# Kernel tuning notes

Measured on AMD Instinct MI355X. Metric: run time of the kernel, lower is better.

## Reference

```python
import jax, jax.numpy as jnp
import numpy as np

HALF_STEP = 0.05
NUM_V = 10  # clamp(floor(0.5/0.05), 2, 1000)
EPS = 1e-6


def _normalize(x):
    return x / (jnp.linalg.norm(x, axis=-1, keepdims=True) + EPS)


def _ragged_structure(edge_points_np):
    # Concrete (numpy) ragged-grid index structure: per-edge horizontal sample
    # counts from edge length, exclusive-cumsum offsets, repeat_interleave ids.
    sp = edge_points_np[:, 0]
    cd = edge_points_np[:, 1] - sp
    cl = np.linalg.norm(cd + EPS, axis=1)
    num_h = np.clip((cl // HALF_STEP).astype(np.int64), 2, 1000)  # [N]
    total_x = int(num_h.sum())
    begin = np.concatenate([[0], np.cumsum(num_h)[:-1]])           # roll-based exclusive cumsum
    eid_x = np.repeat(np.arange(len(num_h)), num_h)                # [total_x] edge id per x-sample
    pos_x = np.arange(total_x) - begin[eid_x]                      # dx integer position within edge
    eid = np.repeat(eid_x, NUM_V)                                  # [P] edge id per sample point
    pos_x_full = np.repeat(pos_x, NUM_V).astype(np.float32)        # coords_x integer part
    dy_idx = np.tile(np.arange(NUM_V), total_x).astype(np.float32) # coords_y integer part
    denom_full = np.repeat((num_h - 1)[eid_x], NUM_V).astype(np.float32)
    return (jnp.asarray(eid), jnp.asarray(pos_x_full), jnp.asarray(denom_full),
            jnp.asarray(dy_idx))


def _sample_img(img, uv):
    # img [1,3,H,W]; uv [P,2] in [0,1) -> bilinear sample (align_corners style)
    im = img[0]
    H, W = im.shape[1], im.shape[2]
    x = uv[:, 0] * (W - 1)
    y = uv[:, 1] * (H - 1)
    x0 = jnp.floor(x).astype(jnp.int32)
    y0 = jnp.floor(y).astype(jnp.int32)
    x1 = jnp.clip(x0 + 1, 0, W - 1)
    y1 = jnp.clip(y0 + 1, 0, H - 1)
    wx = (x - x0)[None]
    wy = (y - y0)[None]
    g = lambda yy, xx: im[:, yy, xx]  # [3,P] gather
    out = (g(y0, x0) * (1 - wx) * (1 - wy) + g(y0, x1) * wx * (1 - wy)
           + g(y1, x0) * (1 - wx) * wy + g(y1, x1) * wx * wy)
    return out.T  # [P,3]


def _forward(edge_points, intrinsic1, intrinsic2, extrinsic1, extrinsic2,
             rgb1, rgb2, eid, pos_x, denom, dy_idx):
    start = edge_points[:, 0]
    cur_dir = edge_points[:, 1] - start
    next_dir = edge_points[:, 3] - edge_points[:, 1]
    prev_dir = edge_points[:, 0] - edge_points[:, 2]
    cur_len = jnp.linalg.norm(cur_dir + EPS, axis=1)
    cur_dir = cur_dir / cur_len[:, None]
    cur_normal = _normalize(jnp.cross(cur_dir, next_dir))
    flip = cur_normal[:, 2] > 0  # dot with (0,0,1) > 0 -> flip sign
    cur_normal = jnp.where(flip[:, None], -cur_normal, cur_normal)
    cur_up = _normalize(jnp.cross(cur_normal, cur_dir))
    prev_normal = _normalize(jnp.cross(prev_dir, cur_dir))

    # ragged per-edge sample grid (repeat_interleave realized via gather on eid)
    coords_x = pos_x / denom * cur_len[eid]          # [P]
    coords_y = dy_idx / (NUM_V - 1) * 0.5            # [P]
    pts = (cur_dir[eid] * coords_x[:, None]
           + cur_up[eid] * coords_y[:, None]
           + start[eid])                              # [P,3]

    # view 1 projection + bilinear sample
    uv1 = pts @ intrinsic1.T
    uv1 = jnp.clip(uv1[:, :2] / uv1[:, 2:3], 0.0, 0.999999)
    s1 = _sample_img(rgb1, uv1)

    # view 2: K2_homog @ E2 @ inv(E1) applied to homogeneous points
    K2h = jnp.eye(4, dtype=pts.dtype).at[:3, :3].set(intrinsic2)
    T = K2h @ extrinsic2 @ jnp.linalg.inv(extrinsic1)
    ph = jnp.concatenate([pts, jnp.ones_like(pts[:, :1])], axis=1)
    uv2 = ph @ T.T
    uv2 = jnp.clip(uv2[:, :2] / uv2[:, 2:3], 0.0, 0.999999)
    s2 = _sample_img(rgb2, uv2)

    similarity_loss = jnp.mean((s1 - s2) ** 2)
    normal_loss = jnp.mean(1.0 - jnp.sum(cur_normal * prev_normal, axis=1)) / 2.0
    obs_normal = _normalize(jnp.cross(edge_points[:, 0], edge_points[:, 1]))
    snp = jnp.minimum(jnp.abs(jnp.sum(cur_up * obs_normal, axis=1)), 0.5)
    normalization_loss = jnp.mean(1.0 - snp / 0.5)
    return jnp.stack([similarity_loss, normal_loss, normalization_loss])


def setup_inputs() -> dict:
    key = jax.random.key(0)
    k0, k1, k2 = jax.random.split(key, 3)
    N, H, W = 10000, 1500, 2000
    # camera-space edge endpoints/neighbors, pushed in front of the camera
    edge_points = jax.random.normal(k0, (N, 4, 3), dtype=jnp.float32) \
        + jnp.array([0.0, 0.0, 6.0], dtype=jnp.float32)
    intrinsic1 = jnp.array([[0.3, 0.0, 0.5], [0.0, 0.3, 0.5], [0.0, 0.0, 1.0]],
                           dtype=jnp.float32)
    intrinsic2 = intrinsic1
    extrinsic1 = jnp.eye(4, dtype=jnp.float32)
    extrinsic2 = jnp.eye(4, dtype=jnp.float32).at[:3, 3].set(
        jnp.array([0.1, 0.0, 0.0], dtype=jnp.float32))
    rgb1 = jax.random.uniform(k1, (1, 3, H, W), dtype=jnp.float32)
    rgb2 = jax.random.uniform(k2, (1, 3, H, W), dtype=jnp.float32)
    return {"edge_points": edge_points, "intrinsic1": intrinsic1,
            "intrinsic2": intrinsic2, "extrinsic1": extrinsic1,
            "extrinsic2": extrinsic2, "rgb1": rgb1, "rgb2": rgb2}


def reference(edge_points, intrinsic1, intrinsic2, extrinsic1, extrinsic2,
              rgb1, rgb2):
    eid, pos_x, denom, dy_idx = _ragged_structure(np.asarray(edge_points))
    return _forward(edge_points, intrinsic1, intrinsic2, extrinsic1,
                    extrinsic2, rgb1, rgb2, eid, pos_x, denom, dy_idx)
```

## Files before the change

### kernel.cpp

```cpp
#include <hip/hip_runtime.h>
#include <math.h>

#define EPSF 1e-6f
#define NUM_V 10
#define W_IMG 2000
#define H_IMG 1500
#define HW_IMG (W_IMG * H_IMG)
#define TH_QUAD (H_IMG - 1)
#define SAMPLE_BLOCKS 2048
#define NPART (SAMPLE_BLOCKS * 4)
#define MAX_CHUNKS 80
#define RPB_P 2048

struct Ctrl {
    int cursor;
    int pad0, pad1, pad2;
    double accNL;
    double accZL;
    double accC;
};

__device__ __forceinline__ void cross3(const float a[3], const float b[3], float c[3]) {
    c[0] = a[1] * b[2] - a[2] * b[1];
    c[1] = a[2] * b[0] - a[0] * b[2];
    c[2] = a[0] * b[1] - a[1] * b[0];
}
__device__ __forceinline__ float dot3(const float a[3], const float b[3]) {
    return a[0] * b[0] + a[1] * b[1] + a[2] * b[2];
}
__device__ __forceinline__ float norm3(const float a[3]) {
    return sqrtf(a[0] * a[0] + a[1] * a[1] + a[2] * a[2]);
}

__device__ void make_T(const float* __restrict__ K2, const float* __restrict__ E1,
                       const float* __restrict__ E2, float* __restrict__ T) {
    float M[4][8];
    for (int i = 0; i < 4; ++i)
        for (int j = 0; j < 4; ++j) {
            M[i][j] = E1[i * 4 + j];
            M[i][j + 4] = (i == j) ? 1.f : 0.f;
        }
    for (int col = 0; col < 4; ++col) {
        int piv = col;
        float best = fabsf(M[col][col]);
        for (int r = col + 1; r < 4; ++r) {
            float v = fabsf(M[r][col]);
            if (v > best) { best = v; piv = r; }
        }
        if (piv != col)
            for (int j = 0; j < 8; ++j) {
                float t = M[col][j]; M[col][j] = M[piv][j]; M[piv][j] = t;
            }
        float d = 1.f / M[col][col];
        for (int j = 0; j < 8; ++j) M[col][j] *= d;
        for (int r = 0; r < 4; ++r) {
            if (r == col) continue;
            float f = M[r][col];
            for (int j = 0; j < 8; ++j) M[r][j] -= f * M[col][j];
        }
    }
    float E[4][4];
    for (int i = 0; i < 4; ++i)
        for (int j = 0; j < 4; ++j) {
            float s = 0.f;
            for (int k = 0; k < 4; ++k) s += E2[i * 4 + k] * M[k][j + 4];
            E[i][j] = s;
        }
    for (int i = 0; i < 4; ++i)
        for (int j = 0; j < 4; ++j) {
            float s;
            if (i < 3) {
                s = 0.f;
                for (int k = 0; k < 3; ++k) s += K2[i * 3 + k] * E[k][j];
            } else {
                s = E[3][j];
            }
            T[i * 4 + j] = s;
        }
}

__device__ __forceinline__ unsigned quant565(float r, float g, float b) {
    unsigned r5 = (unsigned)fmaf(r, 31.f, 0.5f);
    unsigned g6 = (unsigned)fmaf(g, 63.f, 0.5f);
    unsigned b5 = (unsigned)fmaf(b, 31.f, 0.5f);
    return (r5 << 11) | (g6 << 5) | b5;
}

__global__ __launch_bounds__(256, 8) void prep_kernel(
    const float* __restrict__ ep, int N, int GB,
    const float* __restrict__ K2v, const float* __restrict__ E1, const float* __restrict__ E2,
    const float* __restrict__ rgb1, const float* __restrict__ rgb2,
    float* __restrict__ T, Ctrl* __restrict__ ctrl,
    float4* __restrict__ geo, unsigned* __restrict__ sched,
    unsigned* __restrict__ t1, unsigned* __restrict__ t2) {
    const int b = blockIdx.x;
    if (b < RPB_P) {
        const int gpi = TH_QUAD * (W_IMG / 4);
        for (int t = b * 256 + threadIdx.x; t < 2 * gpi; t += RPB_P * 256) {
            const int img = t >= gpi;
            const int g = t - img * gpi;
            const int y = g / (W_IMG / 4);
            const int x = (g - y * (W_IMG / 4)) * 4;
            const float* src = img ? rgb2 : rgb1;
            unsigned* dst = img ? t2 : t1;
            float4 r0[3], r1[3];
#pragma unroll
            for (int c = 0; c < 3; ++c) {
                const float* bp = src + (size_t)c * HW_IMG + (size_t)y * W_IMG + x;
                r0[c] = *(const float4*)bp;
                r1[c] = *(const float4*)(bp + W_IMG);
            }
            const float* f0r = (const float*)&r0[0]; const float* f1r = (const float*)&r1[0];
            const float* f0g = (const float*)&r0[1]; const float* f1g = (const float*)&r1[1];
            const float* f0b = (const float*)&r0[2]; const float* f1b = (const float*)&r1[2];
            unsigned w[4];
#pragma unroll
            for (int k = 0; k < 4; ++k) {
                unsigned lo = quant565(f0r[k], f0g[k], f0b[k]);
                unsigned hi = quant565(f1r[k], f1g[k], f1b[k]);
                w[k] = lo | (hi << 16);
            }
            *(uint4*)(dst + (size_t)y * W_IMG + x) = make_uint4(w[0], w[1], w[2], w[3]);
        }
        return;
    }
    if (b < RPB_P + GB) {
        const int e = (b - RPB_P) * 256 + threadIdx.x;
        float nl = 0.f, zl = 0.f;
        int cn = 0;
        if (e < N) {
            const float4* P4 = (const float4*)(ep + (size_t)e * 12);
            float4 a4 = P4[0], b4 = P4[1], c4 = P4[2];
            float p0[3] = {a4.x, a4.y, a4.z};
            float p1[3] = {a4.w, b4.x, b4.y};
            float p2[3] = {b4.z, b4.w, c4.x};
            float p3[3] = {c4.y, c4.z, c4.w};
            float cd[3] = {p1[0] - p0[0], p1[1] - p0[1], p1[2] - p0[2]};
            float nd[3] = {p3[0] - p1[0], p3[1] - p1[1], p3[2] - p1[2]};
            float pd[3] = {p0[0] - p2[0], p0[1] - p2[1], p0[2] - p2[2]};
            float ce[3] = {cd[0] + EPSF, cd[1] + EPSF, cd[2] + EPSF};
            float clen = norm3(ce);
            float dir[3] = {cd[0] / clen, cd[1] / clen, cd[2] / clen};
            float cnv[3];
            cross3(dir, nd, cnv);
            float n1 = norm3(cnv) + EPSF;
            cnv[0] /= n1; cnv[1] /= n1; cnv[2] /= n1;
            if (cnv[2] > 0.f) { cnv[0] = -cnv[0]; cnv[1] = -cnv[1]; cnv[2] = -cnv[2]; }
            float up[3];
            cross3(cnv, dir, up);
            float n2 = norm3(up) + EPSF;
            up[0] /= n2; up[1] /= n2; up[2] /= n2;
            float pn[3];
            cross3(pd, dir, pn);
            float n3 = norm3(pn) + EPSF;
            pn[0] /= n3; pn[1] /= n3; pn[2] /= n3;
            float obs[3];
            cross3(p0, p1, obs);
            float n4 = norm3(obs) + EPSF;
            obs[0] /= n4; obs[1] /= n4; obs[2] /= n4;
            int nh = (int)floorf(clen / 0.05f);
            nh = max(2, min(1000, nh));
            nl = 1.f - dot3(cnv, pn);
            float snp = fminf(fabsf(dot3(up, obs)), 0.5f);
            zl = 1.f - snp * 2.f;
            const int nsamp = nh * NUM_V;
            cn = nsamp;
            geo[3 * e + 0] = make_float4(p0[0], p0[1], p0[2], clen);
            geo[3 * e + 1] = make_float4(dir[0], dir[1], dir[2], (float)(nh - 1));
            geo[3 * e + 2] = make_float4(up[0], up[1], up[2], __int_as_float(nsamp));
            const int nc = (nsamp + 127) / 128;
            const int basee = atomicAdd(&ctrl->cursor, nc);
            const unsigned tag = ((unsigned)e) << 8;
            for (int j = 0; j < nc; ++j) sched[basee + j] = tag | (unsigned)j;
        }
#pragma unroll
        for (int off = 32; off > 0; off >>= 1) {
            nl += __shfl_down(nl, off);
            zl += __shfl_down(zl, off);
            cn += __shfl_down(cn, off);
        }
        if ((threadIdx.x & 63) == 0) {
            atomicAdd(&ctrl->accNL, (double)nl);
            atomicAdd(&ctrl->accZL, (double)zl);
            atomicAdd(&ctrl->accC, (double)cn);
        }
        return;
    }
    if (threadIdx.x == 0) make_T(K2v, E1, E2, T);
}

__device__ __forceinline__ float mse565(unsigned qa0, unsigned qa1, unsigned qb0, unsigned qb1,
                                        float wxa, float wya, float wxb, float wyb) {
    float wa00 = (1.f - wxa) * (1.f - wya), wa01 = wxa * (1.f - wya);
    float wa10 = (1.f - wxa) * wya, wa11 = wxa * wya;
    float wb00 = (1.f - wxb) * (1.f - wyb), wb01 = wxb * (1.f - wyb);
    float wb10 = (1.f - wxb) * wyb, wb11 = wxb * wyb;
    unsigned a00 = qa0 & 0xffffu, a10 = qa0 >> 16, a01 = qa1 & 0xffffu, a11 = qa1 >> 16;
    unsigned b00 = qb0 & 0xffffu, b10 = qb0 >> 16, b01 = qb1 & 0xffffu, b11 = qb1 >> 16;
    float ra = fmaf((float)(a00 >> 11), wa00, fmaf((float)(a01 >> 11), wa01,
               fmaf((float)(a10 >> 11), wa10, (float)(a11 >> 11) * wa11)));
    float rb = fmaf((float)(b00 >> 11), wb00, fmaf((float)(b01 >> 11), wb01,
               fmaf((float)(b10 >> 11), wb10, (float)(b11 >> 11) * wb11)));
    float ga = fmaf((float)((a00 >> 5) & 63u), wa00, fmaf((float)((a01 >> 5) & 63u), wa01,
               fmaf((float)((a10 >> 5) & 63u), wa10, (float)((a11 >> 5) & 63u) * wa11)));
    float gb = fmaf((float)((b00 >> 5) & 63u), wb00, fmaf((float)((b01 >> 5) & 63u), wb01,
               fmaf((float)((b10 >> 5) & 63u), wb10, (float)((b11 >> 5) & 63u) * wb11)));
    float ba = fmaf((float)(a00 & 31u), wa00, fmaf((float)(a01 & 31u), wa01,
               fmaf((float)(a10 & 31u), wa10, (float)(a11 & 31u) * wa11)));
    float bb = fmaf((float)(b00 & 31u), wb00, fmaf((float)(b01 & 31u), wb01,
               fmaf((float)(b10 & 31u), wb10, (float)(b11 & 31u) * wb11)));
    float dr = (ra - rb) * (1.f / 31.f);
    float dg = (ga - gb) * (1.f / 63.f);
    float db = (ba - bb) * (1.f / 31.f);
    return fmaf(dr, dr, fmaf(dg, dg, db * db));
}

__global__ __launch_bounds__(256, 8) void sample_kernel(
    const float4* __restrict__ geo, const float* __restrict__ K1, const float* __restrict__ T,
    const unsigned* __restrict__ im1, const unsigned* __restrict__ im2,
    const unsigned* __restrict__ sched, const int* __restrict__ total_p,
    double* __restrict__ part) {
    const int wid = blockIdx.x * 4 + (threadIdx.x >> 6);
    const int lane = threadIdx.x & 63;
    const int nw = gridDim.x * 4;
    const int total = *total_p;

    const float k00 = K1[0], k01 = K1[1], k02 = K1[2];
    const float k10 = K1[3], k11 = K1[4], k12 = K1[5];
    const float k20 = K1[6], k21 = K1[7], k22 = K1[8];
    const float t00 = T[0], t01 = T[1], t02 = T[2], t03 = T[3];
    const float t10 = T[4], t11 = T[5], t12 = T[6], t13 = T[7];
    const float t20 = T[8], t21 = T[9], t22 = T[10], t23 = T[11];

    float lsum = 0.f;
    for (int base = wid; base < total; base += 2 * nw) {
        const int idxB = base + nw;
        const bool has2 = idxB < total;
        const unsigned sA = (unsigned)__builtin_amdgcn_readfirstlane((int)sched[base]);
        const unsigned sB =
            has2 ? (unsigned)__builtin_amdgcn_readfirstlane((int)sched[idxB]) : sA;
        const int eA = (int)(sA >> 8), kA = (int)(sA & 255u);
        const int eB = (int)(sB >> 8), kB = (int)(sB & 255u);
        const float4 a0 = geo[3 * eA + 0], a1 = geo[3 * eA + 1], a2 = geo[3 * eA + 2];
        const float4 b0 = geo[3 * eB + 0], b1 = geo[3 * eB + 1], b2 = geo[3 * eB + 2];
        const int nsA = __float_as_int(a2.w), nsB = __float_as_int(b2.w);
        const float lodA = a0.w * __builtin_amdgcn_rcpf(a1.w);
        const float lodB = b0.w * __builtin_amdgcn_rcpf(b1.w);

        int off1[4], off2[4];
        float wx1[4], wy1[4], wx2[4], wy2[4];
        bool ok[4];
#pragma unroll
        for (int j = 0; j < 4; ++j) {
            const int d = j >> 1, h = j & 1;
            const float4 g0 = d ? b0 : a0;
            const float4 g1 = d ? b1 : a1;
            const float4 g2 = d ? b2 : a2;
            const int ns = d ? nsB : nsA;
            const int kk = d ? kB : kA;
            const float lod = d ? lodB : lodA;
            const int i = kk * 128 + h * 64 + lane;
            ok[j] = (i < ns) && (d == 0 || has2);
            const int ic = min(i, ns - 1);
            int px = ic / NUM_V;
            int dy = ic - px * NUM_V;
            float cx = (float)px * lod;
            float cy = (float)dy * (0.5f / 9.0f);
            float X = fmaf(g1.x, cx, fmaf(g2.x, cy, g0.x));
            float Y = fmaf(g1.y, cx, fmaf(g2.y, cy, g0.y));
            float Z = fmaf(g1.z, cx, fmaf(g2.z, cy, g0.z));
            float iw1 = __builtin_amdgcn_rcpf(fmaf(k20, X, fmaf(k21, Y, k22 * Z)));
            float u1 = fminf(fmaxf(fmaf(k00, X, fmaf(k01, Y, k02 * Z)) * iw1, 0.f), 0.999999f);
            float v1 = fminf(fmaxf(fmaf(k10, X, fmaf(k11, Y, k12 * Z)) * iw1, 0.f), 0.999999f);
            float iw2 = __builtin_amdgcn_rcpf(fmaf(t20, X, fmaf(t21, Y, fmaf(t22, Z, t23))));
            float u2 = fminf(
                fmaxf(fmaf(t00, X, fmaf(t01, Y, fmaf(t02, Z, t03))) * iw2, 0.f), 0.999999f);
            float v2 = fminf(
                fmaxf(fmaf(t10, X, fmaf(t11, Y, fmaf(t12, Z, t13))) * iw2, 0.f), 0.999999f);
            float xa = u1 * (float)(W_IMG - 1), ya = v1 * (float)(H_IMG - 1);
            float xb = u2 * (float)(W_IMG - 1), yb = v2 * (float)(H_IMG - 1);
            float fxa = floorf(xa), fya = floorf(ya), fxb = floorf(xb), fyb = floorf(yb);
            off1[j] = (int)fya * W_IMG + (int)fxa;
            off2[j] = (int)fyb * W_IMG + (int)fxb;
            wx1[j] = xa - fxa; wy1[j] = ya - fya;
            wx2[j] = xb - fxb; wy2[j] = yb - fyb;
        }
        unsigned q1a[4], q1b[4], q2a[4], q2b[4];
#pragma unroll
        for (int j = 0; j < 4; ++j) { q1a[j] = im1[off1[j]]; q1b[j] = im1[off1[j] + 1]; }
#pragma unroll
        for (int j = 0; j < 4; ++j) { q2a[j] = im2[off2[j]]; q2b[j] = im2[off2[j] + 1]; }
#pragma unroll
        for (int j = 0; j < 4; ++j) {
            float v = mse565(q1a[j], q1b[j], q2a[j], q2b[j], wx1[j], wy1[j], wx2[j], wy2[j]);
            lsum += ok[j] ? v : 0.f;
        }
    }
    double dsum = (double)lsum;
#pragma unroll
    for (int off = 32; off > 0; off >>= 1) dsum += __shfl_down(dsum, off);
    if (lane == 0) part[wid] = dsum;
}

__global__ __launch_bounds__(256) void finalize_kernel(const double* __restrict__ part, int NP,
                                                       const Ctrl* __restrict__ ctrl, int N,
                                                       float* __restrict__ out) {
    __shared__ double s_s[4];
    double s = 0.0;
    for (int i = threadIdx.x; i < NP; i += 256) s += part[i];
#pragma unroll
    for (int off = 32; off > 0; off >>= 1) s += __shfl_down(s, off);
    const int wave = threadIdx.x >> 6;
    if ((threadIdx.x & 63) == 0) s_s[wave] = s;
    __syncthreads();
    if (threadIdx.x == 0) {
        double S = s_s[0] + s_s[1] + s_s[2] + s_s[3];
        double A = ctrl->accNL;
        double B = ctrl->accZL;
        double C = ctrl->accC;
        out[0] = (float)(S / (C * 3.0));
        out[1] = (float)(A / (double)N * 0.5);
        out[2] = (float)(B / (double)N);
    }
}

extern "C" void kernel_launch(void* const* d_in, const int* in_sizes, int n_in, void* d_out,
                              int out_size, void* d_ws, size_t ws_size, hipStream_t stream) {
    const float* ep = (const float*)d_in[0];
    const float* K1 = (const float*)d_in[1];
    const float* K2 = (const float*)d_in[2];
    const float* E1 = (const float*)d_in[3];
    const float* E2 = (const float*)d_in[4];
    const float* rgb1 = (const float*)d_in[5];
    const float* rgb2 = (const float*)d_in[6];
    float* out = (float*)d_out;
    const int N = in_sizes[0] / 12;

    const int GB = (N + 255) / 256;

    char* p = (char*)d_ws;
    float* T = (float*)p;               p += 256;
    Ctrl* ctrl = (Ctrl*)p;              p += 256;
    float4* geo = (float4*)p;           p += (size_t)3 * N * sizeof(float4);
    p = (char*)(((size_t)p + 255) & ~(size_t)255);
    double* part = (double*)p;          p += (size_t)NPART * sizeof(double);
    p = (char*)(((size_t)p + 255) & ~(size_t)255);
    unsigned* sched = (unsigned*)p;     p += (size_t)N * MAX_CHUNKS * sizeof(unsigned);
    p = (char*)(((size_t)p + 255) & ~(size_t)255);
    unsigned* img1 = (unsigned*)p;
    unsigned* img2 = img1 + (size_t)TH_QUAD * W_IMG;

    hipMemsetAsync(ctrl, 0, sizeof(Ctrl), stream);
    prep_kernel<<<RPB_P + GB + 1, 256, 0, stream>>>(ep, N, GB, K2, E1, E2, rgb1, rgb2, T,
                                                    ctrl, geo, sched, img1, img2);
    sample_kernel<<<SAMPLE_BLOCKS, 256, 0, stream>>>(geo, K1, T, img1, img2, sched,
                                                     &ctrl->cursor, part);
    finalize_kernel<<<1, 256, 0, stream>>>(part, NPART, ctrl, N, out);
}
```

Before: 167.5 us.

## Fuse prep, sample and finalize into one persistent kernel with grid barrier

Merges the memset, prep, sample and finalize launches into a single persistent kernel. A software grid barrier built on a global atomic counter separates the prep phase from the sampling phase, and a last-block-done counter runs the final reduction. The last block also resets the global counters, so no memset launch is needed. This removes three launch and inter-kernel gaps, but the barrier depends on all 2040 blocks being resident at once, which can deadlock if occupancy is insufficient, and prep work is now spread across blocks differently.

```diff
diff --git a/kernel.cpp b/kernel.cpp
--- a/kernel.cpp
+++ b/kernel.cpp
@@ -7,18 +7,22 @@
 #define H_IMG 1500
 #define HW_IMG (W_IMG * H_IMG)
 #define TH_QUAD (H_IMG - 1)
-#define SAMPLE_BLOCKS 2048
-#define NPART (SAMPLE_BLOCKS * 4)
+#define NBLK 2040
+#define NPART (NBLK * 4)
 #define MAX_CHUNKS 80
-#define RPB_P 2048
 
 struct Ctrl {
     int cursor;
-    int pad0, pad1, pad2;
+    int pad;
     double accNL;
     double accZL;
     double accC;
 };
+__device__ Ctrl g_ctrl;
+__device__ int g_sync0;
+__device__ int g_sync1;
+__device__ float g_T[16];
+__device__ double g_part[NPART];
 
 __device__ __forceinline__ void cross3(const float a[3], const float b[3], float c[3]) {
     c[0] = a[1] * b[2] - a[2] * b[1];
@@ -86,46 +90,47 @@
     return (r5 << 11) | (g6 << 5) | b5;
 }
 
-__global__ __launch_bounds__(256, 8) void prep_kernel(
+__device__ __forceinline__ float mse565(unsigned qa0, unsigned qa1, unsigned qb0, unsigned qb1,
+                                        float wxa, float wya, float wxb, float wyb) {
+    float wa00 = (1.f - wxa) * (1.f - wya), wa01 = wxa * (1.f - wya);
+    float wa10 = (1.f - wxa) * wya, wa11 = wxa * wya;
+    float wb00 = (1.f - wxb) * (1.f - wyb), wb01 = wxb * (1.f - wyb);
+    float wb10 = (1.f - wxb) * wyb, wb11 = wxb * wyb;
+    unsigned a00 = qa0 & 0xffffu, a10 = qa0 >> 16, a01 = qa1 & 0xffffu, a11 = qa1 >> 16;
+    unsigned b00 = qb0 & 0xffffu, b10 = qb0 >> 16, b01 = qb1 & 0xffffu, b11 = qb1 >> 16;
+    float ra = fmaf((float)(a00 >> 11), wa00, fmaf((float)(a01 >> 11), wa01,
+               fmaf((float)(a10 >> 11), wa10, (float)(a11 >> 11) * wa11)));
+    float rb = fmaf((float)(b00 >> 11), wb00, fmaf((float)(b01 >> 11), wb01,
+               fmaf((float)(b10 >> 11), wb10, (float)(b11 >> 11) * wb11)));
+    float ga = fmaf((float)((a00 >> 5) & 63u), wa00, fmaf((float)((a01 >> 5) & 63u), wa01,
+               fmaf((float)((a10 >> 5) & 63u), wa10, (float)((a11 >> 5) & 63u) * wa11)));
+    float gb = fmaf((float)((b00 >> 5) & 63u), wb00, fmaf((float)((b01 >> 5) & 63u), wb01,
+               fmaf((float)((b10 >> 5) & 63u), wb10, (float)((b11 >> 5) & 63u) * wb11)));
+    float ba = fmaf((float)(a00 & 31u), wa00, fmaf((float)(a01 & 31u), wa01,
+               fmaf((float)(a10 & 31u), wa10, (float)(a11 & 31u) * wa11)));
+    float bb = fmaf((float)(b00 & 31u), wb00, fmaf((float)(b01 & 31u), wb01,
+               fmaf((float)(b10 & 31u), wb10, (float)(b11 & 31u) * wb11)));
+    float dr = (ra - rb) * (1.f / 31.f);
+    float dg = (ga - gb) * (1.f / 63.f);
+    float db = (ba - bb) * (1.f / 31.f);
+    return fmaf(dr, dr, fmaf(dg, dg, db * db));
+}
+
+__global__ __launch_bounds__(256, 8) void mega_kernel(
     const float* __restrict__ ep, int N, int GB,
-    const float* __restrict__ K2v, const float* __restrict__ E1, const float* __restrict__ E2,
+    const float* __restrict__ K1, const float* __restrict__ K2v,
+    const float* __restrict__ E1, const float* __restrict__ E2,
     const float* __restrict__ rgb1, const float* __restrict__ rgb2,
-    float* __restrict__ T, Ctrl* __restrict__ ctrl,
     float4* __restrict__ geo, unsigned* __restrict__ sched,
-    unsigned* __restrict__ t1, unsigned* __restrict__ t2) {
+    unsigned* __restrict__ t1, unsigned* __restrict__ t2,
+    float* __restrict__ out) {
     const int b = blockIdx.x;
-    if (b < RPB_P) {
-        const int gpi = TH_QUAD * (W_IMG / 4);
-        for (int t = b * 256 + threadIdx.x; t < 2 * gpi; t += RPB_P * 256) {
-            const int img = t >= gpi;
-            const int g = t - img * gpi;
-            const int y = g / (W_IMG / 4);
-            const int x = (g - y * (W_IMG / 4)) * 4;
-            const float* src = img ? rgb2 : rgb1;
-            unsigned* dst = img ? t2 : t1;
-            float4 r0[3], r1[3];
-#pragma unroll
-            for (int c = 0; c < 3; ++c) {
-                const float* bp = src + (size_t)c * HW_IMG + (size_t)y * W_IMG + x;
-                r0[c] = *(const float4*)bp;
-                r1[c] = *(const float4*)(bp + W_IMG);
-            }
-            const float* f0r = (const float*)&r0[0]; const float* f1r = (const float*)&r1[0];
-            const float* f0g = (const float*)&r0[1]; const float* f1g = (const float*)&r1[1];
-            const float* f0b = (const float*)&r0[2]; const float* f1b = (const float*)&r1[2];
-            unsigned w[4];
-#pragma unroll
-            for (int k = 0; k < 4; ++k) {
-                unsigned lo = quant565(f0r[k], f0g[k], f0b[k]);
-                unsigned hi = quant565(f1r[k], f1g[k], f1b[k]);
-                w[k] = lo | (hi << 16);
-            }
-            *(uint4*)(dst + (size_t)y * W_IMG + x) = make_uint4(w[0], w[1], w[2], w[3]);
-        }
-        return;
-    }
-    if (b < RPB_P + GB) {
-        const int e = (b - RPB_P) * 256 + threadIdx.x;
+    const int tid = threadIdx.x;
+
+    if (b == NBLK - 1 && tid == 0) make_T(K2v, E1, E2, g_T);
+
+    if (b < GB) {
+        const int e = b * 256 + tid;
         float nl = 0.f, zl = 0.f;
         int cn = 0;
         if (e < N) {
@@ -169,7 +174,7 @@
             geo[3 * e + 1] = make_float4(dir[0], dir[1], dir[2], (float)(nh - 1));
             geo[3 * e + 2] = make_float4(up[0], up[1], up[2], __int_as_float(nsamp));
             const int nc = (nsamp + 127) / 128;
-            const int basee = atomicAdd(&ctrl->cursor, nc);
+            const int basee = atomicAdd(&g_ctrl.cursor, nc);
             const unsigned tag = ((unsigned)e) << 8;
             for (int j = 0; j < nc; ++j) sched[basee + j] = tag | (unsigned)j;
         }
@@ -179,58 +184,63 @@
             zl += __shfl_down(zl, off);
             cn += __shfl_down(cn, off);
         }
-        if ((threadIdx.x & 63) == 0) {
-            atomicAdd(&ctrl->accNL, (double)nl);
-            atomicAdd(&ctrl->accZL, (double)zl);
-            atomicAdd(&ctrl->accC, (double)cn);
-        }
-        return;
-    }
-    if (threadIdx.x == 0) make_T(K2v, E1, E2, T);
-}
-
-__device__ __forceinline__ float mse565(unsigned qa0, unsigned qa1, unsigned qb0, unsigned qb1,
-                                        float wxa, float wya, float wxb, float wyb) {
-    float wa00 = (1.f - wxa) * (1.f - wya), wa01 = wxa * (1.f - wya);
-    float wa10 = (1.f - wxa) * wya, wa11 = wxa * wya;
-    float wb00 = (1.f - wxb) * (1.f - wyb), wb01 = wxb * (1.f - wyb);
-    float wb10 = (1.f - wxb) * wyb, wb11 = wxb * wyb;
-    unsigned a00 = qa0 & 0xffffu, a10 = qa0 >> 16, a01 = qa1 & 0xffffu, a11 = qa1 >> 16;
-    unsigned b00 = qb0 & 0xffffu, b10 = qb0 >> 16, b01 = qb1 & 0xffffu, b11 = qb1 >> 16;
-    float ra = fmaf((float)(a00 >> 11), wa00, fmaf((float)(a01 >> 11), wa01,
-               fmaf((float)(a10 >> 11), wa10, (float)(a11 >> 11) * wa11)));
-    float rb = fmaf((float)(b00 >> 11), wb00, fmaf((float)(b01 >> 11), wb01,
-               fmaf((float)(b10 >> 11), wb10, (float)(b11 >> 11) * wb11)));
-    float ga = fmaf((float)((a00 >> 5) & 63u), wa00, fmaf((float)((a01 >> 5) & 63u), wa01,
-               fmaf((float)((a10 >> 5) & 63u), wa10, (float)((a11 >> 5) & 63u) * wa11)));
-    float gb = fmaf((float)((b00 >> 5) & 63u), wb00, fmaf((float)((b01 >> 5) & 63u), wb01,
-               fmaf((float)((b10 >> 5) & 63u), wb10, (float)((b11 >> 5) & 63u) * wb11)));
-    float ba = fmaf((float)(a00 & 31u), wa00, fmaf((float)(a01 & 31u), wa01,
-               fmaf((float)(a10 & 31u), wa10, (float)(a11 & 31u) * wa11)));
-    float bb = fmaf((float)(b00 & 31u), wb00, fmaf((float)(b01 & 31u), wb01,
-               fmaf((float)(b10 & 31u), wb10, (float)(b11 & 31u) * wb11)));
-    float dr = (ra - rb) * (1.f / 31.f);
-    float dg = (ga - gb) * (1.f / 63.f);
-    float db = (ba - bb) * (1.f / 31.f);
-    return fmaf(dr, dr, fmaf(dg, dg, db * db));
-}
-
-__global__ __launch_bounds__(256, 8) void sample_kernel(
-    const float4* __restrict__ geo, const float* __restrict__ K1, const float* __restrict__ T,
-    const unsigned* __restrict__ im1, const unsigned* __restrict__ im2,
-    const unsigned* __restrict__ sched, const int* __restrict__ total_p,
-    double* __restrict__ part) {
-    const int wid = blockIdx.x * 4 + (threadIdx.x >> 6);
-    const int lane = threadIdx.x & 63;
-    const int nw = gridDim.x * 4;
-    const int total = *total_p;
+        if ((tid & 63) == 0) {
+            atomicAdd(&g_ctrl.accNL, (double)nl);
+            atomicAdd(&g_ctrl.accZL, (double)zl);
+            atomicAdd(&g_ctrl.accC, (double)cn);
+        }
+    }
+
+    {
+        const int gpi = TH_QUAD * (W_IMG / 4);
+        for (int t = b * 256 + tid; t < 2 * gpi; t += NBLK * 256) {
+            const int img = t >= gpi;
+            const int g = t - img * gpi;
+            const int y = g / (W_IMG / 4);
+            const int x = (g - y * (W_IMG / 4)) * 4;
+            const float* src = img ? rgb2 : rgb1;
+            unsigned* dst = img ? t2 : t1;
+            float4 r0[3], r1[3];
+#pragma unroll
+            for (int c = 0; c < 3; ++c) {
+                const float* bp = src + (size_t)c * HW_IMG + (size_t)y * W_IMG + x;
+                r0[c] = *(const float4*)bp;
+                r1[c] = *(const float4*)(bp + W_IMG);
+            }
+            const float* f0r = (const float*)&r0[0]; const float* f1r = (const float*)&r1[0];
+            const float* f0g = (const float*)&r0[1]; const float* f1g = (const float*)&r1[1];
+            const float* f0b = (const float*)&r0[2]; const float* f1b = (const float*)&r1[2];
+            unsigned w[4];
+#pragma unroll
+            for (int k = 0; k < 4; ++k) {
+                unsigned lo = quant565(f0r[k], f0g[k], f0b[k]);
+                unsigned hi = quant565(f1r[k], f1g[k], f1b[k]);
+                w[k] = lo | (hi << 16);
+            }
+            *(uint4*)(dst + (size_t)y * W_IMG + x) = make_uint4(w[0], w[1], w[2], w[3]);
+        }
+    }
+
+    __syncthreads();
+    if (tid == 0) {
+        __threadfence();
+        __hip_atomic_fetch_add(&g_sync0, 1, __ATOMIC_ACQ_REL, __HIP_MEMORY_SCOPE_AGENT);
+        while (__hip_atomic_load(&g_sync0, __ATOMIC_ACQUIRE, __HIP_MEMORY_SCOPE_AGENT) < NBLK)
+            __builtin_amdgcn_s_sleep(2);
+    }
+    __syncthreads();
+
+    const int wid = b * 4 + (tid >> 6);
+    const int lane = tid & 63;
+    const int nw = NBLK * 4;
+    const int total = g_ctrl.cursor;
 
     const float k00 = K1[0], k01 = K1[1], k02 = K1[2];
     const float k10 = K1[3], k11 = K1[4], k12 = K1[5];
     const float k20 = K1[6], k21 = K1[7], k22 = K1[8];
-    const float t00 = T[0], t01 = T[1], t02 = T[2], t03 = T[3];
-    const float t10 = T[4], t11 = T[5], t12 = T[6], t13 = T[7];
-    const float t20 = T[8], t21 = T[9], t22 = T[10], t23 = T[11];
+    const float t00 = g_T[0], t01 = g_T[1], t02 = g_T[2], t03 = g_T[3];
+    const float t10 = g_T[4], t11 = g_T[5], t12 = g_T[6], t13 = g_T[7];
+    const float t20 = g_T[8], t21 = g_T[9], t22 = g_T[10], t23 = g_T[11];
 
     float lsum = 0.f;
     for (int base = wid; base < total; base += 2 * nw) {
@@ -287,9 +297,9 @@
         }
         unsigned q1a[4], q1b[4], q2a[4], q2b[4];
 #pragma unroll
-        for (int j = 0; j < 4; ++j) { q1a[j] = im1[off1[j]]; q1b[j] = im1[off1[j] + 1]; }
-#pragma unroll
-        for (int j = 0; j < 4; ++j) { q2a[j] = im2[off2[j]]; q2b[j] = im2[off2[j] + 1]; }
+        for (int j = 0; j < 4; ++j) { q1a[j] = t1[off1[j]]; q1b[j] = t1[off1[j] + 1]; }
+#pragma unroll
+        for (int j = 0; j < 4; ++j) { q2a[j] = t2[off2[j]]; q2b[j] = t2[off2[j] + 1]; }
 #pragma unroll
         for (int j = 0; j < 4; ++j) {
             float v = mse565(q1a[j], q1b[j], q2a[j], q2b[j], wx1[j], wy1[j], wx2[j], wy2[j]);
@@ -299,28 +309,41 @@
     double dsum = (double)lsum;
 #pragma unroll
     for (int off = 32; off > 0; off >>= 1) dsum += __shfl_down(dsum, off);
-    if (lane == 0) part[wid] = dsum;
-}
-
-__global__ __launch_bounds__(256) void finalize_kernel(const double* __restrict__ part, int NP,
-                                                       const Ctrl* __restrict__ ctrl, int N,
-                                                       float* __restrict__ out) {
+    if (lane == 0) g_part[wid] = dsum;
+
+    __shared__ int s_last;
     __shared__ double s_s[4];
+    __syncthreads();
+    if (tid == 0) {
+        __threadfence();
+        int prev = __hip_atomic_fetch_add(&g_sync1, 1, __ATOMIC_ACQ_REL,
+                                          __HIP_MEMORY_SCOPE_AGENT);
+        s_last = (prev == NBLK - 1) ? 1 : 0;
+    }
+    __syncthreads();
+    if (!s_last) return;
+
     double s = 0.0;
-    for (int i = threadIdx.x; i < NP; i += 256) s += part[i];
+    for (int i = tid; i < NPART; i += 256) s += g_part[i];
 #pragma unroll
     for (int off = 32; off > 0; off >>= 1) s += __shfl_down(s, off);
-    const int wave = threadIdx.x >> 6;
-    if ((threadIdx.x & 63) == 0) s_s[wave] = s;
-    __syncthreads();
-    if (threadIdx.x == 0) {
+    if ((tid & 63) == 0) s_s[tid >> 6] = s;
+    __syncthreads();
+    if (tid == 0) {
         double S = s_s[0] + s_s[1] + s_s[2] + s_s[3];
-        double A = ctrl->accNL;
-        double B = ctrl->accZL;
-        double C = ctrl->accC;
+        double A = g_ctrl.accNL;
+        double B = g_ctrl.accZL;
+        double C = g_ctrl.accC;
         out[0] = (float)(S / (C * 3.0));
         out[1] = (float)(A / (double)N * 0.5);
         out[2] = (float)(B / (double)N);
+        g_ctrl.cursor = 0;
+        g_ctrl.accNL = 0.0;
+        g_ctrl.accZL = 0.0;
+        g_ctrl.accC = 0.0;
+        __hip_atomic_store(&g_sync0, 0, __ATOMIC_RELAXED, __HIP_MEMORY_SCOPE_AGENT);
+        __hip_atomic_store(&g_sync1, 0, __ATOMIC_RELEASE, __HIP_MEMORY_SCOPE_AGENT);
+        __threadfence();
     }
 }
 
@@ -339,21 +362,13 @@
     const int GB = (N + 255) / 256;
 
     char* p = (char*)d_ws;
-    float* T = (float*)p;               p += 256;
-    Ctrl* ctrl = (Ctrl*)p;              p += 256;
     float4* geo = (float4*)p;           p += (size_t)3 * N * sizeof(float4);
-    p = (char*)(((size_t)p + 255) & ~(size_t)255);
-    double* part = (double*)p;          p += (size_t)NPART * sizeof(double);
     p = (char*)(((size_t)p + 255) & ~(size_t)255);
     unsigned* sched = (unsigned*)p;     p += (size_t)N * MAX_CHUNKS * sizeof(unsigned);
     p = (char*)(((size_t)p + 255) & ~(size_t)255);
     unsigned* img1 = (unsigned*)p;
     unsigned* img2 = img1 + (size_t)TH_QUAD * W_IMG;
 
-    hipMemsetAsync(ctrl, 0, sizeof(Ctrl), stream);
-    prep_kernel<<<RPB_P + GB + 1, 256, 0, stream>>>(ep, N, GB, K2, E1, E2, rgb1, rgb2, T,
-                                                    ctrl, geo, sched, img1, img2);
-    sample_kernel<<<SAMPLE_BLOCKS, 256, 0, stream>>>(geo, K1, T, img1, img2, sched,
-                                                     &ctrl->cursor, part);
-    finalize_kernel<<<1, 256, 0, stream>>>(part, NPART, ctrl, N, out);
-}
+    mega_kernel<<<NBLK, 256, 0, stream>>>(ep, N, GB, K1, K2, E1, E2, rgb1, rgb2,
+                                          geo, sched, img1, img2, out);
+}
```

New measurement: 585.9 us. 250% more time.

## Precompute per-edge projected pixel-space affine coefficients and drop control memset

Applied to the files above, without the earlier changes.

Per-edge geometry is folded with both camera projections (K1 and the precomputed T) and the image scale in the prep kernel. The sampler then evaluates each sample as two small affine combinations plus a reciprocal instead of a 3D point build followed by two full projections. The control block moves to a __device__ global that finalize resets, which removes the hipMemsetAsync launch. In exchange the per-edge record grows from 3 to 6 float4, so the sampler reads more geometry per chunk, and every prep edge block recomputes T into shared memory.

```diff
diff --git a/kernel.cpp b/kernel.cpp
--- a/kernel.cpp
+++ b/kernel.cpp
@@ -11,14 +11,17 @@
 #define NPART (SAMPLE_BLOCKS * 4)
 #define MAX_CHUNKS 80
 #define RPB_P 2048
+#define XCLAMP (0.999999f * (float)(W_IMG - 1))
+#define YCLAMP (0.999999f * (float)(H_IMG - 1))
 
 struct Ctrl {
     int cursor;
-    int pad0, pad1, pad2;
+    int pad;
     double accNL;
     double accZL;
     double accC;
 };
+__device__ Ctrl g_ctrl;
 
 __device__ __forceinline__ void cross3(const float a[3], const float b[3], float c[3]) {
     c[0] = a[1] * b[2] - a[2] * b[1];
@@ -88,9 +91,9 @@
 
 __global__ __launch_bounds__(256, 8) void prep_kernel(
     const float* __restrict__ ep, int N, int GB,
-    const float* __restrict__ K2v, const float* __restrict__ E1, const float* __restrict__ E2,
+    const float* __restrict__ K1, const float* __restrict__ K2v,
+    const float* __restrict__ E1, const float* __restrict__ E2,
     const float* __restrict__ rgb1, const float* __restrict__ rgb2,
-    float* __restrict__ T, Ctrl* __restrict__ ctrl,
     float4* __restrict__ geo, unsigned* __restrict__ sched,
     unsigned* __restrict__ t1, unsigned* __restrict__ t2) {
     const int b = blockIdx.x;
@@ -125,6 +128,9 @@
         return;
     }
     if (b < RPB_P + GB) {
+        __shared__ float sT[16];
+        if (threadIdx.x == 0) make_T(K2v, E1, E2, sT);
+        __syncthreads();
         const int e = (b - RPB_P) * 256 + threadIdx.x;
         float nl = 0.f, zl = 0.f;
         int cn = 0;
@@ -165,11 +171,34 @@
             zl = 1.f - snp * 2.f;
             const int nsamp = nh * NUM_V;
             cn = nsamp;
-            geo[3 * e + 0] = make_float4(p0[0], p0[1], p0[2], clen);
-            geo[3 * e + 1] = make_float4(dir[0], dir[1], dir[2], (float)(nh - 1));
-            geo[3 * e + 2] = make_float4(up[0], up[1], up[2], __int_as_float(nsamp));
+
+            const float lod = clen / (float)(nh - 1);
+            float dlx[3] = {dir[0] * lod, dir[1] * lod, dir[2] * lod};
+            const float cyc = 0.5f / 9.0f;
+            float upc[3] = {up[0] * cyc, up[1] * cyc, up[2] * cyc};
+            const float Wm1 = (float)(W_IMG - 1), Hm1 = (float)(H_IMG - 1);
+            float k0[3] = {K1[0], K1[1], K1[2]};
+            float k1r[3] = {K1[3], K1[4], K1[5]};
+            float k2[3] = {K1[6], K1[7], K1[8]};
+            float T0[3] = {sT[0], sT[1], sT[2]};
+            float T1[3] = {sT[4], sT[5], sT[6]};
+            float T2[3] = {sT[8], sT[9], sT[10]};
+            geo[6 * e + 0] = make_float4(dot3(k0, dlx) * Wm1, dot3(k1r, dlx) * Hm1,
+                                         dot3(k2, dlx), __int_as_float(nsamp));
+            geo[6 * e + 1] = make_float4(dot3(k0, upc) * Wm1, dot3(k1r, upc) * Hm1,
+                                         dot3(k2, upc), 0.f);
+            geo[6 * e + 2] = make_float4(dot3(k0, p0) * Wm1, dot3(k1r, p0) * Hm1,
+                                         dot3(k2, p0), 0.f);
+            geo[6 * e + 3] = make_float4(dot3(T0, dlx) * Wm1, dot3(T1, dlx) * Hm1,
+                                         dot3(T2, dlx), 0.f);
+            geo[6 * e + 4] = make_float4(dot3(T0, upc) * Wm1, dot3(T1, upc) * Hm1,
+                                         dot3(T2, upc), 0.f);
+            geo[6 * e + 5] = make_float4((dot3(T0, p0) + sT[3]) * Wm1,
+                                         (dot3(T1, p0) + sT[7]) * Hm1,
+                                         dot3(T2, p0) + sT[11], 0.f);
+
             const int nc = (nsamp + 127) / 128;
-            const int basee = atomicAdd(&ctrl->cursor, nc);
+            const int basee = atomicAdd(&g_ctrl.cursor, nc);
             const unsigned tag = ((unsigned)e) << 8;
             for (int j = 0; j < nc; ++j) sched[basee + j] = tag | (unsigned)j;
         }
@@ -180,13 +209,11 @@
             cn += __shfl_down(cn, off);
         }
         if ((threadIdx.x & 63) == 0) {
-            atomicAdd(&ctrl->accNL, (double)nl);
-            atomicAdd(&ctrl->accZL, (double)zl);
-            atomicAdd(&ctrl->accC, (double)cn);
-        }
-        return;
-    }
-    if (threadIdx.x == 0) make_T(K2v, E1, E2, T);
+            atomicAdd(&g_ctrl.accNL, (double)nl);
+            atomicAdd(&g_ctrl.accZL, (double)zl);
+            atomicAdd(&g_ctrl.accC, (double)cn);
+        }
+    }
 }
 
 __device__ __forceinline__ float mse565(unsigned qa0, unsigned qa1, unsigned qb0, unsigned qb1,
@@ -216,21 +243,13 @@
 }
 
 __global__ __launch_bounds__(256, 8) void sample_kernel(
-    const float4* __restrict__ geo, const float* __restrict__ K1, const float* __restrict__ T,
+    const float4* __restrict__ geo,
     const unsigned* __restrict__ im1, const unsigned* __restrict__ im2,
-    const unsigned* __restrict__ sched, const int* __restrict__ total_p,
-    double* __restrict__ part) {
+    const unsigned* __restrict__ sched, double* __restrict__ part) {
     const int wid = blockIdx.x * 4 + (threadIdx.x >> 6);
     const int lane = threadIdx.x & 63;
     const int nw = gridDim.x * 4;
-    const int total = *total_p;
-
-    const float k00 = K1[0], k01 = K1[1], k02 = K1[2];
-    const float k10 = K1[3], k11 = K1[4], k12 = K1[5];
-    const float k20 = K1[6], k21 = K1[7], k22 = K1[8];
-    const float t00 = T[0], t01 = T[1], t02 = T[2], t03 = T[3];
-    const float t10 = T[4], t11 = T[5], t12 = T[6], t13 = T[7];
-    const float t20 = T[8], t21 = T[9], t22 = T[10], t23 = T[11];
+    const int total = g_ctrl.cursor;
 
     float lsum = 0.f;
     for (int base = wid; base < total; base += 2 * nw) {
@@ -241,11 +260,9 @@
             has2 ? (unsigned)__builtin_amdgcn_readfirstlane((int)sched[idxB]) : sA;
         const int eA = (int)(sA >> 8), kA = (int)(sA & 255u);
         const int eB = (int)(sB >> 8), kB = (int)(sB & 255u);
-        const float4 a0 = geo[3 * eA + 0], a1 = geo[3 * eA + 1], a2 = geo[3 * eA + 2];
-        const float4 b0 = geo[3 * eB + 0], b1 = geo[3 * eB + 1], b2 = geo[3 * eB + 2];
-        const int nsA = __float_as_int(a2.w), nsB = __float_as_int(b2.w);
-        const float lodA = a0.w * __builtin_amdgcn_rcpf(a1.w);
-        const float lodB = b0.w * __builtin_amdgcn_rcpf(b1.w);
+        const float4* gA = &geo[6 * eA];
+        const float4* gB = &geo[6 * eB];
+        const int nsA = __float_as_int(gA[0].w), nsB = __float_as_int(gB[0].w);
 
         int off1[4], off2[4];
         float wx1[4], wy1[4], wx2[4], wy2[4];
@@ -253,32 +270,29 @@
 #pragma unroll
         for (int j = 0; j < 4; ++j) {
             const int d = j >> 1, h = j & 1;
-            const float4 g0 = d ? b0 : a0;
-            const float4 g1 = d ? b1 : a1;
-            const float4 g2 = d ? b2 : a2;
+            const float4* g = d ? gB : gA;
             const int ns = d ? nsB : nsA;
             const int kk = d ? kB : kA;
-            const float lod = d ? lodB : lodA;
             const int i = kk * 128 + h * 64 + lane;
             ok[j] = (i < ns) && (d == 0 || has2);
             const int ic = min(i, ns - 1);
             int px = ic / NUM_V;
             int dy = ic - px * NUM_V;
-            float cx = (float)px * lod;
-            float cy = (float)dy * (0.5f / 9.0f);
-            float X = fmaf(g1.x, cx, fmaf(g2.x, cy, g0.x));
-            float Y = fmaf(g1.y, cx, fmaf(g2.y, cy, g0.y));
-            float Z = fmaf(g1.z, cx, fmaf(g2.z, cy, g0.z));
-            float iw1 = __builtin_amdgcn_rcpf(fmaf(k20, X, fmaf(k21, Y, k22 * Z)));
-            float u1 = fminf(fmaxf(fmaf(k00, X, fmaf(k01, Y, k02 * Z)) * iw1, 0.f), 0.999999f);
-            float v1 = fminf(fmaxf(fmaf(k10, X, fmaf(k11, Y, k12 * Z)) * iw1, 0.f), 0.999999f);
-            float iw2 = __builtin_amdgcn_rcpf(fmaf(t20, X, fmaf(t21, Y, fmaf(t22, Z, t23))));
-            float u2 = fminf(
-                fmaxf(fmaf(t00, X, fmaf(t01, Y, fmaf(t02, Z, t03))) * iw2, 0.f), 0.999999f);
-            float v2 = fminf(
-                fmaxf(fmaf(t10, X, fmaf(t11, Y, fmaf(t12, Z, t13))) * iw2, 0.f), 0.999999f);
-            float xa = u1 * (float)(W_IMG - 1), ya = v1 * (float)(H_IMG - 1);
-            float xb = u2 * (float)(W_IMG - 1), yb = v2 * (float)(H_IMG - 1);
+            const float fpx = (float)px, fdy = (float)dy;
+            const float4 s0 = g[0], s1 = g[1], s2 = g[2];
+            float u1n = fmaf(fpx, s0.x, fmaf(fdy, s1.x, s2.x));
+            float v1n = fmaf(fpx, s0.y, fmaf(fdy, s1.y, s2.y));
+            float w1  = fmaf(fpx, s0.z, fmaf(fdy, s1.z, s2.z));
+            const float4 s3 = g[3], s4 = g[4], s5 = g[5];
+            float u2n = fmaf(fpx, s3.x, fmaf(fdy, s4.x, s5.x));
+            float v2n = fmaf(fpx, s3.y, fmaf(fdy, s4.y, s5.y));
+            float w2  = fmaf(fpx, s3.z, fmaf(fdy, s4.z, s5.z));
+            float iw1 = __builtin_amdgcn_rcpf(w1);
+            float iw2 = __builtin_amdgcn_rcpf(w2);
+            float xa = fminf(fmaxf(u1n * iw1, 0.f), XCLAMP);
+            float ya = fminf(fmaxf(v1n * iw1, 0.f), YCLAMP);
+            float xb = fminf(fmaxf(u2n * iw2, 0.f), XCLAMP);
+            float yb = fminf(fmaxf(v2n * iw2, 0.f), YCLAMP);
             float fxa = floorf(xa), fya = floorf(ya), fxb = floorf(xb), fyb = floorf(yb);
             off1[j] = (int)fya * W_IMG + (int)fxa;
             off2[j] = (int)fyb * W_IMG + (int)fxb;
@@ -303,8 +317,7 @@
 }
 
 __global__ __launch_bounds__(256) void finalize_kernel(const double* __restrict__ part, int NP,
-                                                       const Ctrl* __restrict__ ctrl, int N,
-                                                       float* __restrict__ out) {
+                                                       int N, float* __restrict__ out) {
     __shared__ double s_s[4];
     double s = 0.0;
     for (int i = threadIdx.x; i < NP; i += 256) s += part[i];
@@ -315,12 +328,16 @@
     __syncthreads();
     if (threadIdx.x == 0) {
         double S = s_s[0] + s_s[1] + s_s[2] + s_s[3];
-        double A = ctrl->accNL;
-        double B = ctrl->accZL;
-        double C = ctrl->accC;
+        double A = g_ctrl.accNL;
+        double B = g_ctrl.accZL;
+        double C = g_ctrl.accC;
         out[0] = (float)(S / (C * 3.0));
         out[1] = (float)(A / (double)N * 0.5);
         out[2] = (float)(B / (double)N);
+        g_ctrl.cursor = 0;
+        g_ctrl.accNL = 0.0;
+        g_ctrl.accZL = 0.0;
+        g_ctrl.accC = 0.0;
     }
 }
 
@@ -339,9 +356,7 @@
     const int GB = (N + 255) / 256;
 
     char* p = (char*)d_ws;
-    float* T = (float*)p;               p += 256;
-    Ctrl* ctrl = (Ctrl*)p;              p += 256;
-    float4* geo = (float4*)p;           p += (size_t)3 * N * sizeof(float4);
+    float4* geo = (float4*)p;           p += (size_t)6 * N * sizeof(float4);
     p = (char*)(((size_t)p + 255) & ~(size_t)255);
     double* part = (double*)p;          p += (size_t)NPART * sizeof(double);
     p = (char*)(((size_t)p + 255) & ~(size_t)255);
@@ -350,10 +365,8 @@
     unsigned* img1 = (unsigned*)p;
     unsigned* img2 = img1 + (size_t)TH_QUAD * W_IMG;
 
-    hipMemsetAsync(ctrl, 0, sizeof(Ctrl), stream);
-    prep_kernel<<<RPB_P + GB + 1, 256, 0, stream>>>(ep, N, GB, K2, E1, E2, rgb1, rgb2, T,
-                                                    ctrl, geo, sched, img1, img2);
-    sample_kernel<<<SAMPLE_BLOCKS, 256, 0, stream>>>(geo, K1, T, img1, img2, sched,
-                                                     &ctrl->cursor, part);
-    finalize_kernel<<<1, 256, 0, stream>>>(part, NPART, ctrl, N, out);
-}
+    prep_kernel<<<RPB_P + GB, 256, 0, stream>>>(ep, N, GB, K1, K2, E1, E2, rgb1, rgb2,
+                                                geo, sched, img1, img2);
+    sample_kernel<<<SAMPLE_BLOCKS, 256, 0, stream>>>(geo, img1, img2, sched, part);
+    finalize_kernel<<<1, 256, 0, stream>>>(part, NPART, N, out);
+}
```

Result: no change. 164.4 us (-1.8%).
